# Performance work log

Measured on AMD Instinct MI355X. Metric: run time of the kernel, lower is better.

## Reference

```python
import jax, jax.numpy as jnp
import numpy as np

HID = 16  # hidden channels of each lifting subnet (P and U)


def _conv(x, W, b):
    # x: [N,1|HID,h,w], W: [O,I,3,3] -> SAME conv, NCHW
    y = jax.lax.conv_general_dilated(x, W, (1, 1), 'SAME',
                                     dimension_numbers=('NCHW', 'OIHW', 'NCHW'))
    return y + b[None, :, None, None]


def _subnet(x, W1, b1, W2, b2):
    return _conv(jax.nn.relu(_conv(x, W1, b1)), W2, b2)


def _lift(L, H, p, u):
    # predict/update lifting step: H -= P(L); L += U(H)
    H = H - _subnet(L, *p)
    L = L + _subnet(H, *u)
    return L, H


def _rgb2yuv(x):
    # [B,3,H,W] -> YUV, then channels folded into batch -> [3B,1,H,W]
    M = jnp.array([[0.299, 0.587, 0.114],
                   [-0.147, -0.289, 0.436],
                   [0.615, -0.515, -0.100]], dtype=x.dtype)
    y = jnp.einsum('cd,bdhw->bchw', M, x)
    B, C, H, W = y.shape
    return y.transpose(1, 0, 2, 3).reshape(C * B, 1, H, W)


def _batch2channel(x, C):
    # [C*B,1,h,w] -> [B,C,h,w]  (inverse of the batch-fold above)
    CB, _, h, w = x.shape
    B = CB // C
    return x.reshape(C, B, h, w).transpose(1, 0, 2, 3)


def setup_inputs():
    key = jax.random.key(0)
    ks = jax.random.split(key, 5)
    B, H, W = 8, 512, 512
    x = jax.random.normal(ks[0], (B, 3, H, W), jnp.float32)

    def w(k, shape, fan):
        return jax.random.normal(k, shape, jnp.float32) * (1.0 / np.sqrt(fan))

    Wp1 = w(ks[1], (HID, 1, 3, 3), 9)
    bp1 = jnp.zeros((HID,), jnp.float32)
    Wp2 = w(ks[2], (1, HID, 3, 3), 9 * HID)
    bp2 = jnp.zeros((1,), jnp.float32)
    Wu1 = w(ks[3], (HID, 1, 3, 3), 9)
    bu1 = jnp.zeros((HID,), jnp.float32)
    Wu2 = w(ks[4], (1, HID, 3, 3), 9 * HID)
    bu2 = jnp.zeros((1,), jnp.float32)
    return dict(x=x, Wp1=Wp1, bp1=bp1, Wp2=Wp2, bp2=bp2,
                Wu1=Wu1, bu1=bu1, Wu2=Wu2, bu2=bu2)


def reference(x, Wp1, bp1, Wp2, bp2, Wu1, bu1, Wu2, bu2):
    p = (Wp1, bp1, Wp2, bp2)
    u = (Wu1, bu1, Wu2, bu2)
    C = x.shape[1]  # 3
    y = _rgb2yuv(x)                              # [3B,1,H,W]
    # level-1 vertical split + lifting
    L, Hb = y[:, :, 0::2, :], y[:, :, 1::2, :]   # [3B,1,H/2,W]
    L, Hb = _lift(L, Hb, p, u)
    # horizontal split of L
    Lt = L.transpose(0, 1, 3, 2)                 # [3B,1,W,H/2]
    LL, HL = Lt[:, :, 0::2, :], Lt[:, :, 1::2, :]
    LL, HL = _lift(LL, HL, p, u)
    LL = LL.transpose(0, 1, 3, 2)                # [3B,1,H/2,W/2]
    HL = HL.transpose(0, 1, 3, 2)
    # horizontal split of H
    Ht = Hb.transpose(0, 1, 3, 2)
    LH, HH = Ht[:, :, 0::2, :], Ht[:, :, 1::2, :]
    LH, HH = _lift(LH, HH, p, u)
    LH = LH.transpose(0, 1, 3, 2)
    HH = HH.transpose(0, 1, 3, 2)
    return jnp.concatenate([_batch2channel(t, C) for t in (LL, HL, LH, HH)],
                           axis=1)                # [B,12,H/2,W/2]
```

## Files before the change

kernel.cpp:

```cpp
#include <hip/hip_runtime.h>


#define P1 (24*256*512)

template<int MODE>
__global__ __launch_bounds__(256, 3) void k_subnet(
    const float* __restrict__ xp, float* __restrict__ ws, float* __restrict__ outp,
    const float* __restrict__ W1, const float* __restrict__ B1,
    const float* __restrict__ W2, const float* __restrict__ B2)
{
  constexpr int  IW    = (MODE <= 1) ? 512 : 256;
  constexpr int  HW    = 256 * IW;
  constexpr float sign = (MODE == 0 || MODE == 2) ? -1.f : 1.f;
  constexpr int  TRANS = (MODE >= 2) ? 1 : 0;

  __shared__ __align__(16) float sIn[68*68];
  __shared__ __align__(16) float sW[16*24];

  const int z     = blockIdx.z;
  const int n     = (MODE >= 2) ? (z % 24) : z;
  const int which = (MODE >= 2) ? (z / 24) : 0;
  const int c_ = n >> 3, b_ = n & 7;
  const int x0 = blockIdx.x * 64, y0 = blockIdx.y * 64;
  const int tid = threadIdx.x;

  float* Lw = ws;
  float* Hw = ws + P1;

  for (int i = tid; i < 16*24; i += 256) {
    int cc = i / 24, j = i - cc*24;
    float v = 0.f;
    if (j < 9)                  { int jt = TRANS ? ((j%3)*3 + j/3) : j; v = W1[cc*9 + jt]; }
    else if (j >= 12 && j < 21) { int k = j - 12; int jt = TRANS ? ((k%3)*3 + k/3) : k; v = W2[cc*9 + jt]; }
    else if (j == 21)           v = B1[cc];
    sW[i] = v;
  }

  float m0 = 0.f, m1 = 0.f, m2 = 0.f;
  if (MODE == 0) {
    m0 = (c_==0) ? 0.299f : ((c_==1) ? -0.147f :  0.615f);
    m1 = (c_==0) ? 0.587f : ((c_==1) ? -0.289f : -0.515f);
    m2 = (c_==0) ? 0.114f : ((c_==1) ?  0.436f : -0.100f);
  }
  for (int i = tid; i < 68*68; i += 256) {
    int ly = i / 68, lx = i - ly*68;
    int gy = y0 + ly - 2, gx = x0 + lx - 2;
    float v = 0.f;
    if ((unsigned)gy < 256u && (unsigned)gx < (unsigned)IW) {
      if (MODE == 0) {
        const float* xb = xp + ((long)b_*3*512 + 2*gy)*512 + gx;
        v = m0*xb[0] + m1*xb[512*512] + m2*xb[2*512*512];
      } else if (MODE == 1) {
        v = Hw[(long)n*HW + gy*IW + gx];
      } else if (MODE == 2) {
        const float* src = (which ? Hw : Lw) + (long)n*(256*512);
        v = src[gy*512 + 2*gx];
      } else {
        const float* src = outp + (long)(b_*12 + (which?9:3) + c_)*(256*256);
        v = src[gy*256 + gx];
      }
    }
    sIn[i] = v;
  }
  __syncthreads();

  const int tx = tid & 15, ty = tid >> 4;
  const int oy = y0 + ty*4, ox = x0 + tx*4;

  if (MODE == 0) {
    float* Lp = Lw + (long)n*HW;
#pragma unroll
    for (int r = 0; r < 4; ++r) {
      const int base = (ty*4 + r + 2)*68 + tx*4 + 2;
      float4 v = make_float4(sIn[base], sIn[base+1], sIn[base+2], sIn[base+3]);
      *(float4*)&Lp[(oy + r)*IW + ox] = v;
    }
  }

  float4 iov[4];
  if (MODE == 0) {
#pragma unroll
    for (int r = 0; r < 4; ++r) {
      const float* xb = xp + ((long)b_*3*512 + (2*(oy+r)+1))*512 + ox;
      float4 rr = *(const float4*)&xb[0];
      float4 gg = *(const float4*)&xb[512*512];
      float4 bb = *(const float4*)&xb[2*512*512];
      iov[r] = make_float4(m0*rr.x + m1*gg.x + m2*bb.x,
                           m0*rr.y + m1*gg.y + m2*bb.y,
                           m0*rr.z + m1*gg.z + m2*bb.z,
                           m0*rr.w + m1*gg.w + m2*bb.w);
    }
  } else if (MODE == 1) {
    const float* src = Lw + (long)n*HW;
#pragma unroll
    for (int r = 0; r < 4; ++r) iov[r] = *(const float4*)&src[(oy+r)*IW + ox];
  } else if (MODE == 2) {
    const float* src = (which ? Hw : Lw) + (long)n*(256*512);
#pragma unroll
    for (int r = 0; r < 4; ++r) {
      float4 a = *(const float4*)&src[(oy+r)*512 + 2*ox];
      float4 b = *(const float4*)&src[(oy+r)*512 + 2*ox + 4];
      iov[r] = make_float4(a.y, a.w, b.y, b.w);
    }
  } else {
    const float* src = (which ? Hw : Lw) + (long)n*(256*512);
#pragma unroll
    for (int r = 0; r < 4; ++r) {
      float4 a = *(const float4*)&src[(oy+r)*512 + 2*ox];
      float4 b = *(const float4*)&src[(oy+r)*512 + 2*ox + 4];
      iov[r] = make_float4(a.x, a.z, b.x, b.z);
    }
  }
  float b2 = B2[0];

  float in_reg[8][8];
#pragma unroll
  for (int rr = 0; rr < 8; ++rr) {
    const float4* p = (const float4*)&sIn[(ty*4 + rr)*68 + tx*4];
    float4 a = p[0], b = p[1];
    in_reg[rr][0]=a.x; in_reg[rr][1]=a.y; in_reg[rr][2]=a.z; in_reg[rr][3]=a.w;
    in_reg[rr][4]=b.x; in_reg[rr][5]=b.y; in_reg[rr][6]=b.z; in_reg[rr][7]=b.w;
  }

  bool  rowv[6];
  float colm[6];
#pragma unroll
  for (int k = 0; k < 6; ++k) {
    rowv[k] = ((unsigned)(oy + k - 1) < 256u);
    colm[k] = ((unsigned)(ox + k - 1) < (unsigned)IW) ? 1.f : 0.f;
  }

  auto ldsW = [&](int cc, float* w) {
    const float4* p = (const float4*)&sW[cc*24];
    float4 q0=p[0], q1=p[1], q2=p[2], q3=p[3], q4=p[4], q5=p[5];
    w[0]=q0.x; w[1]=q0.y; w[2]=q0.z; w[3]=q0.w;
    w[4]=q1.x; w[5]=q1.y; w[6]=q1.z; w[7]=q1.w;
    w[8]=q2.x;
    w[9]=q3.x; w[10]=q3.y; w[11]=q3.z; w[12]=q3.w;
    w[13]=q4.x; w[14]=q4.y; w[15]=q4.z; w[16]=q4.w;
    w[17]=q5.x;
    w[18]=q5.y;
  };

  float acc[4][4] = {{0,0,0,0},{0,0,0,0},{0,0,0,0},{0,0,0,0}};
  float wcur[19];
  ldsW(0, wcur);

#pragma unroll 1
  for (int c = 0; c < 16; ++c) {
    float wnxt[19];
    ldsW((c+1) & 15, wnxt);

    float b1r[6];
#pragma unroll
    for (int k = 0; k < 6; ++k) b1r[k] = rowv[k] ? wcur[18] : -3.0e38f;

#pragma unroll
    for (int hy = 0; hy < 6; ++hy) {
      float h[6];
#pragma unroll
      for (int hx = 0; hx < 6; ++hx) {
        float s = b1r[hy];
#pragma unroll
        for (int dy = 0; dy < 3; ++dy)
#pragma unroll
          for (int dx = 0; dx < 3; ++dx)
            s = fmaf(wcur[dy*3+dx], in_reg[hy+dy][hx+dx], s);
        h[hx] = fmaxf(s, 0.f) * colm[hx];
      }
#pragma unroll
      for (int dy = 0; dy < 3; ++dy) {
        int r = hy - dy;
        if (r >= 0 && r < 4) {
#pragma unroll
          for (int cx = 0; cx < 4; ++cx)
#pragma unroll
            for (int dx = 0; dx < 3; ++dx)
              acc[r][cx] = fmaf(wcur[9 + dy*3 + dx], h[cx+dx], acc[r][cx]);
        }
      }
    }
#pragma unroll
    for (int k = 0; k < 19; ++k) wcur[k] = wnxt[k];
  }

  float* dst;
  if      (MODE == 0) dst = Hw + (long)n*HW;
  else if (MODE == 1) dst = Lw + (long)n*HW;
  else if (MODE == 2) dst = outp + (long)(b_*12 + (which?9:3) + c_)*(256*256);
  else                dst = outp + (long)(b_*12 + (which?6:0) + c_)*(256*256);

#pragma unroll
  for (int r = 0; r < 4; ++r) {
    float4 v;
    v.x = iov[r].x + sign * (acc[r][0] + b2);
    v.y = iov[r].y + sign * (acc[r][1] + b2);
    v.z = iov[r].z + sign * (acc[r][2] + b2);
    v.w = iov[r].w + sign * (acc[r][3] + b2);
    *(float4*)&dst[(oy + r)*IW + ox] = v;
  }
}

extern "C" void kernel_launch(void* const* d_in, const int* in_sizes, int n_in,
                              void* d_out, int out_size, void* d_ws, size_t ws_size,
                              hipStream_t stream) {
  const float* x   = (const float*)d_in[0];
  const float* Wp1 = (const float*)d_in[1];
  const float* bp1 = (const float*)d_in[2];
  const float* Wp2 = (const float*)d_in[3];
  const float* bp2 = (const float*)d_in[4];
  const float* Wu1 = (const float*)d_in[5];
  const float* bu1 = (const float*)d_in[6];
  const float* Wu2 = (const float*)d_in[7];
  const float* bu2 = (const float*)d_in[8];
  float* out = (float*)d_out;
  float* ws  = (float*)d_ws;

  k_subnet<0><<<dim3(8,4,24), 256, 0, stream>>>(x, ws, out, Wp1, bp1, Wp2, bp2);
  k_subnet<1><<<dim3(8,4,24), 256, 0, stream>>>(x, ws, out, Wu1, bu1, Wu2, bu2);
  k_subnet<2><<<dim3(4,4,48), 256, 0, stream>>>(x, ws, out, Wp1, bp1, Wp2, bp2);
  k_subnet<3><<<dim3(4,4,48), 256, 0, stream>>>(x, ws, out, Wu1, bu1, Wu2, bu2);
}
```

Measured before the change: 291.8 us.

## Compute subnet convolutions in packed fp16 with smaller 64x32 tiles

Rewrites the fused two-layer conv inner loop to use packed half2 FMAs. It builds odd-offset pairs with alignbit and applies relu with v_pk_max_f16, while partial sums are flushed to fp32 every four channels. The tile shrinks to 64x32 with 2 output rows per thread, the grid doubles and the occupancy hint rises to 4. In MODE 0 the even rows of L are now written during the halo load. This roughly halves ALU instruction count and register/LDS footprint, at the cost of reduced precision in the hidden activations, which may exceed the tolerance.

```diff
diff --git a/kernel.cpp b/kernel.cpp
--- a/kernel.cpp
+++ b/kernel.cpp
@@ -1,10 +1,23 @@
 #include <hip/hip_runtime.h>
+#include <hip/hip_fp16.h>
 
 
 #define P1 (24*256*512)
 
+__device__ __forceinline__ __half2 oddpair(__half2 a, __half2 b) {
+  unsigned ua = __builtin_bit_cast(unsigned, a), ub = __builtin_bit_cast(unsigned, b);
+  unsigned r = __builtin_amdgcn_alignbit(ub, ua, 16);
+  return __builtin_bit_cast(__half2, r);
+}
+
+__device__ __forceinline__ __half2 relu2(__half2 s) {
+  unsigned u = __builtin_bit_cast(unsigned, s), r;
+  asm("v_pk_max_f16 %0, %1, 0" : "=v"(r) : "v"(u));
+  return __builtin_bit_cast(__half2, r);
+}
+
 template<int MODE>
-__global__ __launch_bounds__(256, 3) void k_subnet(
+__global__ __launch_bounds__(256, 4) void k_subnet(
     const float* __restrict__ xp, float* __restrict__ ws, float* __restrict__ outp,
     const float* __restrict__ W1, const float* __restrict__ B1,
     const float* __restrict__ W2, const float* __restrict__ B2)
@@ -14,26 +27,26 @@
   constexpr float sign = (MODE == 0 || MODE == 2) ? -1.f : 1.f;
   constexpr int  TRANS = (MODE >= 2) ? 1 : 0;
 
-  __shared__ __align__(16) float sIn[68*68];
-  __shared__ __align__(16) float sW[16*24];
+  __shared__ __align__(16) __half2 sW[16*20];
+  __shared__ __align__(16) __half  sIn[36*70];
 
   const int z     = blockIdx.z;
   const int n     = (MODE >= 2) ? (z % 24) : z;
   const int which = (MODE >= 2) ? (z / 24) : 0;
   const int c_ = n >> 3, b_ = n & 7;
-  const int x0 = blockIdx.x * 64, y0 = blockIdx.y * 64;
+  const int x0 = blockIdx.x * 64, y0 = blockIdx.y * 32;
   const int tid = threadIdx.x;
-
   float* Lw = ws;
   float* Hw = ws + P1;
 
-  for (int i = tid; i < 16*24; i += 256) {
-    int cc = i / 24, j = i - cc*24;
+  for (int i = tid; i < 320; i += 256) {
+    int cc = i / 20, j = i - cc*20;
     float v = 0.f;
-    if (j < 9)                  { int jt = TRANS ? ((j%3)*3 + j/3) : j; v = W1[cc*9 + jt]; }
-    else if (j >= 12 && j < 21) { int k = j - 12; int jt = TRANS ? ((k%3)*3 + k/3) : k; v = W2[cc*9 + jt]; }
-    else if (j == 21)           v = B1[cc];
-    sW[i] = v;
+    if (j < 9)       { int jt = TRANS ? ((j%3)*3 + j/3) : j; v = W1[cc*9 + jt]; }
+    else if (j == 9) v = B1[cc];
+    else if (j < 19) { int k = j - 10; int jt = TRANS ? ((k%3)*3 + k/3) : k; v = W2[cc*9 + jt]; }
+    __half h = __float2half(v);
+    sW[i] = __halves2half2(h, h);
   }
 
   float m0 = 0.f, m1 = 0.f, m2 = 0.f;
@@ -42,161 +55,170 @@
     m1 = (c_==0) ? 0.587f : ((c_==1) ? -0.289f : -0.515f);
     m2 = (c_==0) ? 0.114f : ((c_==1) ?  0.436f : -0.100f);
   }
-  for (int i = tid; i < 68*68; i += 256) {
+  for (int i = tid; i < 36*68; i += 256) {
     int ly = i / 68, lx = i - ly*68;
     int gy = y0 + ly - 2, gx = x0 + lx - 2;
     float v = 0.f;
     if ((unsigned)gy < 256u && (unsigned)gx < (unsigned)IW) {
       if (MODE == 0) {
         const float* xb = xp + ((long)b_*3*512 + 2*gy)*512 + gx;
-        v = m0*xb[0] + m1*xb[512*512] + m2*xb[2*512*512];
+        v = m0*xb[0] + m1*xb[262144] + m2*xb[524288];
+        Lw[(long)n*HW + gy*IW + gx] = v;
       } else if (MODE == 1) {
         v = Hw[(long)n*HW + gy*IW + gx];
       } else if (MODE == 2) {
-        const float* src = (which ? Hw : Lw) + (long)n*(256*512);
-        v = src[gy*512 + 2*gx];
+        const float* s = (which ? Hw : Lw) + (long)n*(256*512);
+        v = s[gy*512 + 2*gx];
       } else {
-        const float* src = outp + (long)(b_*12 + (which?9:3) + c_)*(256*256);
-        v = src[gy*256 + gx];
-      }
-    }
-    sIn[i] = v;
+        const float* s = outp + (long)(b_*12 + (which?9:3) + c_)*65536;
+        v = s[gy*256 + gx];
+      }
+    }
+    sIn[ly*70 + lx] = __float2half(v);
   }
   __syncthreads();
 
   const int tx = tid & 15, ty = tid >> 4;
-  const int oy = y0 + ty*4, ox = x0 + tx*4;
-
+  const int oy = y0 + ty*2, ox = x0 + tx*4;
+
+  __half2 E[6][4], O[6][3];
+#pragma unroll
+  for (int r = 0; r < 6; ++r) {
+    const __half2* row = (const __half2*)&sIn[(ty*2 + r)*70 + tx*4];
+    E[r][0] = row[0]; E[r][1] = row[1]; E[r][2] = row[2]; E[r][3] = row[3];
+    O[r][0] = oddpair(E[r][0], E[r][1]);
+    O[r][1] = oddpair(E[r][1], E[r][2]);
+    O[r][2] = oddpair(E[r][2], E[r][3]);
+  }
+
+  const bool edgex = (x0 == 0) || (x0 + 64 == IW);
+  bool rowok[4];
+#pragma unroll
+  for (int k = 0; k < 4; ++k) rowok[k] = ((unsigned)(oy - 1 + k) < 256u);
+  __half2 mE[3];
+  if (edgex) {
+#pragma unroll
+    for (int p = 0; p < 3; ++p) {
+      float a = ((unsigned)(ox - 1 + 2*p) < (unsigned)IW) ? 1.f : 0.f;
+      float b = ((unsigned)(ox     + 2*p) < (unsigned)IW) ? 1.f : 0.f;
+      mE[p] = __halves2half2(__float2half(a), __float2half(b));
+    }
+  }
+
+  const __half2 zero2 = __halves2half2(__float2half(0.f), __float2half(0.f));
+  const __half2 negb  = __halves2half2(__float2half(-60000.f), __float2half(-60000.f));
+
+  float   ACCF[2][4] = {{0,0,0,0},{0,0,0,0}};
+  __half2 ACC2[2][2] = {{zero2, zero2},{zero2, zero2}};
+
+#pragma unroll 1
+  for (int c = 0; c < 16; ++c) {
+    __half2 wv[20];
+    const float4* wq = (const float4*)&sW[c*20];
+#pragma unroll
+    for (int q = 0; q < 5; ++q) {
+      float4 f = wq[q];
+      __half2 ph[4];
+      ph[0] = __builtin_bit_cast(__half2, f.x);
+      ph[1] = __builtin_bit_cast(__half2, f.y);
+      ph[2] = __builtin_bit_cast(__half2, f.z);
+      ph[3] = __builtin_bit_cast(__half2, f.w);
+      wv[4*q+0] = ph[0]; wv[4*q+1] = ph[1]; wv[4*q+2] = ph[2]; wv[4*q+3] = ph[3];
+    }
+    __half2 bias[4];
+#pragma unroll
+    for (int k = 0; k < 4; ++k) bias[k] = rowok[k] ? wv[9] : negb;
+
+#pragma unroll
+    for (int k = 0; k < 4; ++k) {
+      __half2 HE[3];
+#pragma unroll
+      for (int p = 0; p < 3; ++p) {
+        __half2 s = bias[k];
+#pragma unroll
+        for (int dy = 0; dy < 3; ++dy) {
+          s = __hfma2(wv[dy*3+0], E[k+dy][p],   s);
+          s = __hfma2(wv[dy*3+1], O[k+dy][p],   s);
+          s = __hfma2(wv[dy*3+2], E[k+dy][p+1], s);
+        }
+        HE[p] = relu2(s);
+      }
+      if (edgex) {
+        HE[0] = __hmul2(HE[0], mE[0]);
+        HE[1] = __hmul2(HE[1], mE[1]);
+        HE[2] = __hmul2(HE[2], mE[2]);
+      }
+      __half2 HO0 = oddpair(HE[0], HE[1]);
+      __half2 HO1 = oddpair(HE[1], HE[2]);
+#pragma unroll
+      for (int dy = 0; dy < 3; ++dy) {
+        const int r = k - dy;
+        if (r == 0 || r == 1) {
+#pragma unroll
+          for (int cp = 0; cp < 2; ++cp) {
+            __half2 a = ACC2[r][cp];
+            a = __hfma2(wv[10+dy*3+0], HE[cp],          a);
+            a = __hfma2(wv[10+dy*3+1], (cp ? HO1 : HO0), a);
+            a = __hfma2(wv[10+dy*3+2], HE[cp+1],        a);
+            ACC2[r][cp] = a;
+          }
+        }
+      }
+    }
+    if ((c & 3) == 3) {
+#pragma unroll
+      for (int r = 0; r < 2; ++r)
+#pragma unroll
+        for (int cp = 0; cp < 2; ++cp) {
+          ACCF[r][2*cp]   += __low2float(ACC2[r][cp]);
+          ACCF[r][2*cp+1] += __high2float(ACC2[r][cp]);
+          ACC2[r][cp] = zero2;
+        }
+    }
+  }
+
+  const float b2 = B2[0];
+  float4 iov[2];
   if (MODE == 0) {
-    float* Lp = Lw + (long)n*HW;
-#pragma unroll
-    for (int r = 0; r < 4; ++r) {
-      const int base = (ty*4 + r + 2)*68 + tx*4 + 2;
-      float4 v = make_float4(sIn[base], sIn[base+1], sIn[base+2], sIn[base+3]);
-      *(float4*)&Lp[(oy + r)*IW + ox] = v;
-    }
-  }
-
-  float4 iov[4];
-  if (MODE == 0) {
-#pragma unroll
-    for (int r = 0; r < 4; ++r) {
+#pragma unroll
+    for (int r = 0; r < 2; ++r) {
       const float* xb = xp + ((long)b_*3*512 + (2*(oy+r)+1))*512 + ox;
       float4 rr = *(const float4*)&xb[0];
-      float4 gg = *(const float4*)&xb[512*512];
-      float4 bb = *(const float4*)&xb[2*512*512];
+      float4 gg = *(const float4*)&xb[262144];
+      float4 bb = *(const float4*)&xb[524288];
       iov[r] = make_float4(m0*rr.x + m1*gg.x + m2*bb.x,
                            m0*rr.y + m1*gg.y + m2*bb.y,
                            m0*rr.z + m1*gg.z + m2*bb.z,
                            m0*rr.w + m1*gg.w + m2*bb.w);
     }
   } else if (MODE == 1) {
-    const float* src = Lw + (long)n*HW;
-#pragma unroll
-    for (int r = 0; r < 4; ++r) iov[r] = *(const float4*)&src[(oy+r)*IW + ox];
-  } else if (MODE == 2) {
-    const float* src = (which ? Hw : Lw) + (long)n*(256*512);
-#pragma unroll
-    for (int r = 0; r < 4; ++r) {
-      float4 a = *(const float4*)&src[(oy+r)*512 + 2*ox];
-      float4 b = *(const float4*)&src[(oy+r)*512 + 2*ox + 4];
-      iov[r] = make_float4(a.y, a.w, b.y, b.w);
-    }
+    const float* s = Lw + (long)n*HW;
+#pragma unroll
+    for (int r = 0; r < 2; ++r) iov[r] = *(const float4*)&s[(oy+r)*IW + ox];
   } else {
-    const float* src = (which ? Hw : Lw) + (long)n*(256*512);
-#pragma unroll
-    for (int r = 0; r < 4; ++r) {
-      float4 a = *(const float4*)&src[(oy+r)*512 + 2*ox];
-      float4 b = *(const float4*)&src[(oy+r)*512 + 2*ox + 4];
-      iov[r] = make_float4(a.x, a.z, b.x, b.z);
-    }
-  }
-  float b2 = B2[0];
-
-  float in_reg[8][8];
-#pragma unroll
-  for (int rr = 0; rr < 8; ++rr) {
-    const float4* p = (const float4*)&sIn[(ty*4 + rr)*68 + tx*4];
-    float4 a = p[0], b = p[1];
-    in_reg[rr][0]=a.x; in_reg[rr][1]=a.y; in_reg[rr][2]=a.z; in_reg[rr][3]=a.w;
-    in_reg[rr][4]=b.x; in_reg[rr][5]=b.y; in_reg[rr][6]=b.z; in_reg[rr][7]=b.w;
-  }
-
-  bool  rowv[6];
-  float colm[6];
-#pragma unroll
-  for (int k = 0; k < 6; ++k) {
-    rowv[k] = ((unsigned)(oy + k - 1) < 256u);
-    colm[k] = ((unsigned)(ox + k - 1) < (unsigned)IW) ? 1.f : 0.f;
-  }
-
-  auto ldsW = [&](int cc, float* w) {
-    const float4* p = (const float4*)&sW[cc*24];
-    float4 q0=p[0], q1=p[1], q2=p[2], q3=p[3], q4=p[4], q5=p[5];
-    w[0]=q0.x; w[1]=q0.y; w[2]=q0.z; w[3]=q0.w;
-    w[4]=q1.x; w[5]=q1.y; w[6]=q1.z; w[7]=q1.w;
-    w[8]=q2.x;
-    w[9]=q3.x; w[10]=q3.y; w[11]=q3.z; w[12]=q3.w;
-    w[13]=q4.x; w[14]=q4.y; w[15]=q4.z; w[16]=q4.w;
-    w[17]=q5.x;
-    w[18]=q5.y;
-  };
-
-  float acc[4][4] = {{0,0,0,0},{0,0,0,0},{0,0,0,0},{0,0,0,0}};
-  float wcur[19];
-  ldsW(0, wcur);
-
-#pragma unroll 1
-  for (int c = 0; c < 16; ++c) {
-    float wnxt[19];
-    ldsW((c+1) & 15, wnxt);
-
-    float b1r[6];
-#pragma unroll
-    for (int k = 0; k < 6; ++k) b1r[k] = rowv[k] ? wcur[18] : -3.0e38f;
-
-#pragma unroll
-    for (int hy = 0; hy < 6; ++hy) {
-      float h[6];
-#pragma unroll
-      for (int hx = 0; hx < 6; ++hx) {
-        float s = b1r[hy];
-#pragma unroll
-        for (int dy = 0; dy < 3; ++dy)
-#pragma unroll
-          for (int dx = 0; dx < 3; ++dx)
-            s = fmaf(wcur[dy*3+dx], in_reg[hy+dy][hx+dx], s);
-        h[hx] = fmaxf(s, 0.f) * colm[hx];
-      }
-#pragma unroll
-      for (int dy = 0; dy < 3; ++dy) {
-        int r = hy - dy;
-        if (r >= 0 && r < 4) {
-#pragma unroll
-          for (int cx = 0; cx < 4; ++cx)
-#pragma unroll
-            for (int dx = 0; dx < 3; ++dx)
-              acc[r][cx] = fmaf(wcur[9 + dy*3 + dx], h[cx+dx], acc[r][cx]);
-        }
-      }
-    }
-#pragma unroll
-    for (int k = 0; k < 19; ++k) wcur[k] = wnxt[k];
+    const float* s = (which ? Hw : Lw) + (long)n*(256*512);
+#pragma unroll
+    for (int r = 0; r < 2; ++r) {
+      float4 a = *(const float4*)&s[(oy+r)*512 + 2*ox];
+      float4 b = *(const float4*)&s[(oy+r)*512 + 2*ox + 4];
+      iov[r] = (MODE == 2) ? make_float4(a.y, a.w, b.y, b.w)
+                           : make_float4(a.x, a.z, b.x, b.z);
+    }
   }
 
   float* dst;
   if      (MODE == 0) dst = Hw + (long)n*HW;
   else if (MODE == 1) dst = Lw + (long)n*HW;
-  else if (MODE == 2) dst = outp + (long)(b_*12 + (which?9:3) + c_)*(256*256);
-  else                dst = outp + (long)(b_*12 + (which?6:0) + c_)*(256*256);
-
-#pragma unroll
-  for (int r = 0; r < 4; ++r) {
+  else if (MODE == 2) dst = outp + (long)(b_*12 + (which?9:3) + c_)*65536;
+  else                dst = outp + (long)(b_*12 + (which?6:0) + c_)*65536;
+
+#pragma unroll
+  for (int r = 0; r < 2; ++r) {
     float4 v;
-    v.x = iov[r].x + sign * (acc[r][0] + b2);
-    v.y = iov[r].y + sign * (acc[r][1] + b2);
-    v.z = iov[r].z + sign * (acc[r][2] + b2);
-    v.w = iov[r].w + sign * (acc[r][3] + b2);
+    v.x = iov[r].x + sign * (ACCF[r][0] + b2);
+    v.y = iov[r].y + sign * (ACCF[r][1] + b2);
+    v.z = iov[r].z + sign * (ACCF[r][2] + b2);
+    v.w = iov[r].w + sign * (ACCF[r][3] + b2);
     *(float4*)&dst[(oy + r)*IW + ox] = v;
   }
 }
@@ -216,8 +238,8 @@
   float* out = (float*)d_out;
   float* ws  = (float*)d_ws;
 
-  k_subnet<0><<<dim3(8,4,24), 256, 0, stream>>>(x, ws, out, Wp1, bp1, Wp2, bp2);
-  k_subnet<1><<<dim3(8,4,24), 256, 0, stream>>>(x, ws, out, Wu1, bu1, Wu2, bu2);
-  k_subnet<2><<<dim3(4,4,48), 256, 0, stream>>>(x, ws, out, Wp1, bp1, Wp2, bp2);
-  k_subnet<3><<<dim3(4,4,48), 256, 0, stream>>>(x, ws, out, Wu1, bu1, Wu2, bu2);
-}
+  k_subnet<0><<<dim3(8,8,24), 256, 0, stream>>>(x, ws, out, Wp1, bp1, Wp2, bp2);
+  k_subnet<1><<<dim3(8,8,24), 256, 0, stream>>>(x, ws, out, Wu1, bu1, Wu2, bu2);
+  k_subnet<2><<<dim3(4,8,48), 256, 0, stream>>>(x, ws, out, Wp1, bp1, Wp2, bp2);
+  k_subnet<3><<<dim3(4,8,48), 256, 0, stream>>>(x, ws, out, Wu1, bu1, Wu2, bu2);
+}
```

New measurement: 260.6 us. 10.7% less time.
